# Kernel tuning notes

Hardware: AMD Instinct MI355X
Metric: run time of the kernel (lower is better)

## Reference

```python
import jax, jax.numpy as jnp
import numpy as np

B, T, E = 4, 2048, 1024
H = 16
HS = E // H  # head_size = d_model // num_heads, d_model == E here
D_FF = 4 * E
EPS = 1e-5


def _layernorm(x, g, b):
    mu = jnp.mean(x, axis=-1, keepdims=True)
    var = jnp.var(x, axis=-1, keepdims=True)
    return (x - mu) * jax.lax.rsqrt(var + EPS) * g + b


def setup_inputs() -> dict:
    key = jax.random.key(0)
    ks = jax.random.split(key, 12)
    s_e = 1.0 / np.sqrt(E)
    s_ff = 1.0 / np.sqrt(D_FF)
    return {
        "x": jax.random.normal(ks[0], (B, T, E), jnp.float32),
        "ln1_g": jnp.ones((E,), jnp.float32),
        "ln1_b": jnp.zeros((E,), jnp.float32),
        "Wq": jax.random.normal(ks[1], (E, E), jnp.float32) * s_e,
        "bq": jnp.zeros((E,), jnp.float32),
        "Wk": jax.random.normal(ks[2], (E, E), jnp.float32) * s_e,
        "bk": jnp.zeros((E,), jnp.float32),
        "Wv": jax.random.normal(ks[3], (E, E), jnp.float32) * s_e,
        "bv": jnp.zeros((E,), jnp.float32),
        "Wp": jax.random.normal(ks[4], (E, E), jnp.float32) * s_e,
        "bp": jnp.zeros((E,), jnp.float32),
        "ln2_g": jnp.ones((E,), jnp.float32),
        "ln2_b": jnp.zeros((E,), jnp.float32),
        "W1": jax.random.normal(ks[5], (E, D_FF), jnp.float32) * s_e,
        "b1": jnp.zeros((D_FF,), jnp.float32),
        "W2": jax.random.normal(ks[6], (D_FF, E), jnp.float32) * s_ff,
        "b2": jnp.zeros((E,), jnp.float32),
    }


def reference(x, ln1_g, ln1_b, Wq, bq, Wk, bk, Wv, bv, Wp, bp,
              ln2_g, ln2_b, W1, b1, W2, b2):
    # --- attention sublayer ---
    h = _layernorm(x, ln1_g, ln1_b)                      # [B,T,E]
    q = (h @ Wq + bq).reshape(B, T, H, HS)
    k = (h @ Wk + bk).reshape(B, T, H, HS)
    v = (h @ Wv + bv).reshape(B, T, H, HS)
    scores = jnp.einsum('bqhd,bkhd->bhqk', q, k) * (HS ** -0.5)  # [B,H,T,T]
    causal = jnp.tril(jnp.ones((T, T), bool))
    scores = jnp.where(causal, scores, -jnp.inf)
    w = jax.nn.softmax(scores, axis=-1)
    attn = jnp.einsum('bhqk,bkhd->bqhd', w, v).reshape(B, T, H * HS)
    x = x + attn @ Wp + bp
    # --- FFN sublayer ---
    h2 = _layernorm(x, ln2_g, ln2_b)
    x = x + jax.nn.relu(h2 @ W1 + b1) @ W2 + b2
    return x
```

## Files before the change

kernel.cpp:

```cpp
#include <hip/hip_runtime.h>
#include <hip/hip_bf16.h>

#define B_ 4
#define T_ 2048
#define E_ 1024
#define H_ 16
#define HS_ 64
#define DFF_ 4096
#define M_ (B_ * T_)
#define LDQ_ (3 * E_)

typedef __bf16 bf16_t;
typedef __bf16 bf16x4 __attribute__((ext_vector_type(4)));
typedef __bf16 bf16x8 __attribute__((ext_vector_type(8)));
typedef float f32x4 __attribute__((ext_vector_type(4)));

#define AS1 __attribute__((address_space(1)))
#define AS3 __attribute__((address_space(3)))

__device__ __forceinline__ void gload_lds16(const void* g, void* l) {
  __builtin_amdgcn_global_load_lds((AS1 void*)(g), (AS3 void*)(l), 16, 0, 0);
}

__global__ __launch_bounds__(256) void wtrans_kernel(
    const float* __restrict__ W, bf16_t* __restrict__ Wt, int Krows, int Ncols) {
  __shared__ float tile[32][33];
  int tx = threadIdx.x, ty = threadIdx.y;
  int n0 = blockIdx.x * 32, k0 = blockIdx.y * 32;
#pragma unroll
  for (int i = 0; i < 32; i += 8)
    tile[ty + i][tx] = W[(long)(k0 + ty + i) * Ncols + n0 + tx];
  __syncthreads();
#pragma unroll
  for (int i = 0; i < 32; i += 8)
    Wt[(long)(n0 + ty + i) * Krows + k0 + tx] = (bf16_t)tile[tx][ty + i];
}

__global__ __launch_bounds__(256) void bcat_kernel(const float* a, const float* b,
                                                   const float* c, float* o) {
  int i = blockIdx.x * 256 + threadIdx.x;
  o[i] = i < 1024 ? a[i] : (i < 2048 ? b[i - 1024] : c[i - 2048]);
}

__global__ __launch_bounds__(256) void layernorm_kernel(
    const float* __restrict__ in, const float* __restrict__ g,
    const float* __restrict__ b, bf16_t* __restrict__ out) {
  int row = blockIdx.x;
  int tid = threadIdx.x;
  const float4* inr = (const float4*)(in + (long)row * E_);
  float4 v = inr[tid];
  float s = v.x + v.y + v.z + v.w;
  float ss = v.x * v.x + v.y * v.y + v.z * v.z + v.w * v.w;
#pragma unroll
  for (int o = 32; o; o >>= 1) {
    s += __shfl_xor(s, o);
    ss += __shfl_xor(ss, o);
  }
  __shared__ float red[8];
  int wv = tid >> 6;
  if ((tid & 63) == 0) {
    red[wv] = s;
    red[4 + wv] = ss;
  }
  __syncthreads();
  s = red[0] + red[1] + red[2] + red[3];
  ss = red[4] + red[5] + red[6] + red[7];
  float mu = s * (1.f / E_);
  float var = ss * (1.f / E_) - mu * mu;
  float rs = rsqrtf(var + 1e-5f);
  int ci = tid * 4;
  float4 gv = *(const float4*)(g + ci);
  float4 bv = *(const float4*)(b + ci);
  long o0 = (long)row * E_ + ci;
  out[o0 + 0] = (bf16_t)((v.x - mu) * rs * gv.x + bv.x);
  out[o0 + 1] = (bf16_t)((v.y - mu) * rs * gv.y + bv.y);
  out[o0 + 2] = (bf16_t)((v.z - mu) * rs * gv.z + bv.z);
  out[o0 + 3] = (bf16_t)((v.w - mu) * rs * gv.w + bv.w);
}

template <int MODE>
__global__ __launch_bounds__(256, 2) void gemm_bt_kernel(
    const bf16_t* __restrict__ A, const bf16_t* __restrict__ Bt,
    const float* __restrict__ bias, const float* __restrict__ resid,
    void* __restrict__ out, int N, int K) {
  __shared__ bf16_t As[2][128 * 64];
  __shared__ bf16_t Bs[2][128 * 64];
  const int tid = threadIdx.x;
  const int lane = tid & 63;
  const int wave = tid >> 6;
  const int wr = wave >> 1, wc = wave & 1;
  const int quad = lane >> 4, l16 = lane & 15;
  const int id = blockIdx.y * gridDim.x + blockIdx.x;
  const int xcd = id & 7;
  const int k_ = id >> 3;
  const int bxr = k_ % gridDim.x;
  const int byr = (k_ / gridDim.x) * 8 + xcd;
  const long rowBase = (long)byr * 128;
  const long colBase = (long)bxr * 128;

  f32x4 acc[4][4] = {};

  auto stage = [&](int buf, int k0) {
#pragma unroll
    for (int i = 0; i < 4; ++i) {
      int c = i * 256 + tid;
      int row = c >> 3;
      int gcol = ((c & 7) ^ (row & 7)) * 8;
      gload_lds16(&A[(rowBase + row) * K + k0 + gcol],
                  &As[buf][(i * 256 + wave * 64) * 8]);
      gload_lds16(&Bt[(colBase + row) * K + k0 + gcol],
                  &Bs[buf][(i * 256 + wave * 64) * 8]);
    }
  };

  stage(0, 0);
  __syncthreads();

  for (int k0 = 0; k0 < K; k0 += 64) {
    const int cur = (k0 >> 6) & 1;
    if (k0 + 64 < K) stage(cur ^ 1, k0 + 64);
#pragma unroll
    for (int kk = 0; kk < 2; ++kk) {
      bf16x8 af[4], bfr[4];
#pragma unroll
      for (int i = 0; i < 4; ++i) {
        int rowA = wr * 64 + i * 16 + l16;
        af[i] = *(const bf16x8*)&As[cur][(rowA * 8 + ((quad + 4 * kk) ^ (rowA & 7))) * 8];
        int rowB = wc * 64 + i * 16 + l16;
        bfr[i] = *(const bf16x8*)&Bs[cur][(rowB * 8 + ((quad + 4 * kk) ^ (rowB & 7))) * 8];
      }
#pragma unroll
      for (int mi = 0; mi < 4; ++mi)
#pragma unroll
        for (int ni = 0; ni < 4; ++ni)
          acc[mi][ni] = __builtin_amdgcn_mfma_f32_16x16x32_bf16(
              af[mi], bfr[ni], acc[mi][ni], 0, 0, 0);
    }
    __syncthreads();
  }

#pragma unroll
  for (int mi = 0; mi < 4; ++mi) {
#pragma unroll
    for (int ni = 0; ni < 4; ++ni) {
      int colg = (int)colBase + wc * 64 + ni * 16 + l16;
      float bv = bias[colg];
#pragma unroll
      for (int r = 0; r < 4; ++r) {
        long rowg = rowBase + wr * 64 + mi * 16 + quad * 4 + r;
        float v = acc[mi][ni][r] + bv;
        long idx = rowg * N + colg;
        if (MODE == 0) {
          ((bf16_t*)out)[idx] = (bf16_t)v;
        } else if (MODE == 1) {
          ((float*)out)[idx] = v + resid[idx];
        } else {
          ((bf16_t*)out)[idx] = (bf16_t)fmaxf(v, 0.f);
        }
      }
    }
  }
}

__global__ __launch_bounds__(256) void vtrans_kernel(
    const bf16_t* __restrict__ qkv, bf16_t* __restrict__ vt) {
  __shared__ bf16_t tile[32][33];
  int tx = threadIdx.x, ty = threadIdx.y;
  int t0 = blockIdx.x * 32;
  int d0 = (blockIdx.y & 1) * 32;
  int bh = blockIdx.y >> 1;
  int b = bh >> 4, hh = bh & 15;
#pragma unroll
  for (int i = 0; i < 32; i += 8)
    tile[ty + i][tx] =
        qkv[(long)(b * T_ + t0 + ty + i) * LDQ_ + 2 * E_ + hh * HS_ + d0 + tx];
  __syncthreads();
#pragma unroll
  for (int i = 0; i < 32; i += 8)
    vt[((long)bh * HS_ + d0 + ty + i) * T_ + t0 + tx] = tile[tx][ty + i];
}

__global__ __launch_bounds__(256) void flash_attn_kernel(
    const bf16_t* __restrict__ qkv, const bf16_t* __restrict__ vt,
    bf16_t* __restrict__ attn, bf16_t* __restrict__ Opart,
    float* __restrict__ mlpart) {
  int gx = blockIdx.x;
  int ti = 0, sp = 0;
  for (int t = 0; t < 16; ++t) {
    int ns = t / 6 + 1;
    if (gx < ns) { ti = t; sp = gx; break; }
    gx -= ns;
  }
  const int nsplit = ti / 6 + 1;
  const int totIt = 2 * (ti + 1);
  const int jbeg = 12 * sp;
  const int jend = min(jbeg + 12, totIt);

  const int tid = threadIdx.x;
  const int lane = tid & 63, wave = tid >> 6;
  const int quad = lane >> 4, l16 = lane & 15;
  const int bh = blockIdx.y, b = bh >> 4, hh = bh & 15;
  const int q0 = ti * 128;
  const int qw = q0 + wave * 32;

  __shared__ __align__(16) bf16_t Ks[64][72];
  __shared__ __align__(16) bf16_t Vs[64][72];
  __shared__ __align__(16) bf16_t Ps[4][16][72];

  const bf16_t* qb = qkv;
  const bf16_t* kb = qkv + E_;

  bf16x8 aq[2][2];
#pragma unroll
  for (int s = 0; s < 2; ++s) {
    long base = (long)(b * T_ + qw + s * 16 + l16) * LDQ_ + hh * HS_ + quad * 8;
    aq[s][0] = *(const bf16x8*)&qb[base];
    aq[s][1] = *(const bf16x8*)&qb[base + 32];
#pragma unroll
    for (int e = 0; e < 8; ++e) {
      aq[s][0][e] = (bf16_t)((float)aq[s][0][e] * 0.125f);
      aq[s][1][e] = (bf16_t)((float)aq[s][1][e] * 0.125f);
    }
  }

  f32x4 o[2][4] = {};
  float lsum[2] = {};

  const int srow = tid >> 3;
  const int scol = (tid & 7) * 8;

  for (int j = jbeg; j < jend; ++j) {
    int kv0 = j * 64;
#pragma unroll
    for (int p = 0; p < 2; ++p) {
      int row = p * 32 + srow;
      *(uint4*)&Ks[row][scol] =
          *(const uint4*)&kb[(long)(b * T_ + kv0 + row) * LDQ_ + hh * HS_ + scol];
      *(uint4*)&Vs[row][scol] =
          *(const uint4*)&vt[((long)bh * HS_ + row) * T_ + kv0 + scol];
    }
    __syncthreads();

#pragma unroll
    for (int s = 0; s < 2; ++s) {
      int qs = qw + s * 16;
      if (kv0 <= qs + 15) {
        f32x4 sc[4];
#pragma unroll
        for (int sub = 0; sub < 4; ++sub) {
          f32x4 t = {};
          t = __builtin_amdgcn_mfma_f32_16x16x32_bf16(
              *(const bf16x8*)&Ks[sub * 16 + l16][quad * 8], aq[s][0], t, 0, 0, 0);
          t = __builtin_amdgcn_mfma_f32_16x16x32_bf16(
              *(const bf16x8*)&Ks[sub * 16 + l16][32 + quad * 8], aq[s][1], t, 0, 0, 0);
          sc[sub] = t;
        }
        if (kv0 + 63 > qs) {
          int qcol = qs + l16;
#pragma unroll
          for (int sub = 0; sub < 4; ++sub)
#pragma unroll
            for (int r = 0; r < 4; ++r) {
              int kvrow = kv0 + sub * 16 + quad * 4 + r;
              if (kvrow > qcol) sc[sub][r] = -INFINITY;
            }
        }
        float part = 0.f;
#pragma unroll
        for (int sub = 0; sub < 4; ++sub) {
#pragma unroll
          for (int r = 0; r < 4; ++r) sc[sub][r] = __expf(sc[sub][r]);
          part += (sc[sub][0] + sc[sub][1]) + (sc[sub][2] + sc[sub][3]);
        }
        lsum[s] += part;
#pragma unroll
        for (int sub = 0; sub < 4; ++sub) {
          bf16x4 pk;
#pragma unroll
          for (int r = 0; r < 4; ++r) pk[r] = (bf16_t)sc[sub][r];
          *(bf16x4*)&Ps[wave][l16][sub * 16 + quad * 4] = pk;
        }
        bf16x8 ap0 = *(const bf16x8*)&Ps[wave][l16][quad * 8];
        bf16x8 ap1 = *(const bf16x8*)&Ps[wave][l16][32 + quad * 8];
#pragma unroll
        for (int nt = 0; nt < 4; ++nt) {
          o[s][nt] = __builtin_amdgcn_mfma_f32_16x16x32_bf16(
              *(const bf16x8*)&Vs[nt * 16 + l16][quad * 8], ap0, o[s][nt], 0, 0, 0);
          o[s][nt] = __builtin_amdgcn_mfma_f32_16x16x32_bf16(
              *(const bf16x8*)&Vs[nt * 16 + l16][32 + quad * 8], ap1, o[s][nt], 0, 0, 0);
        }
      }
    }
    __syncthreads();
  }

  float lval[2];
#pragma unroll
  for (int s = 0; s < 2; ++s) {
    float v = lsum[s];
    v += __shfl_xor(v, 16);
    v += __shfl_xor(v, 32);
    lval[s] = v;
  }

  if (nsplit == 1) {
#pragma unroll
    for (int s = 0; s < 2; ++s) {
      float inv = 1.f / lval[s];
      long rowg = (long)b * T_ + qw + s * 16 + l16;
#pragma unroll
      for (int nt = 0; nt < 4; ++nt) {
        bf16x4 pk;
#pragma unroll
        for (int r = 0; r < 4; ++r) pk[r] = (bf16_t)(o[s][nt][r] * inv);
        *(bf16x4*)&attn[rowg * E_ + hh * HS_ + nt * 16 + quad * 4] = pk;
      }
    }
  } else {
    int idx = (ti < 12) ? (ti - 6) * 2 + sp : 12 + (ti - 12) * 3 + sp;
    long slot = (long)bh * 24 + idx;
    bf16_t* op = Opart + slot * (128 * 64);
    float* ml = mlpart + slot * 256;
#pragma unroll
    for (int s = 0; s < 2; ++s) {
      float inv = 1.f / lval[s];
      int rloc = wave * 32 + s * 16 + l16;
#pragma unroll
      for (int nt = 0; nt < 4; ++nt) {
        bf16x4 pk;
#pragma unroll
        for (int r = 0; r < 4; ++r) pk[r] = (bf16_t)(o[s][nt][r] * inv);
        *(bf16x4*)&op[rloc * 64 + nt * 16 + quad * 4] = pk;
      }
      if (quad == 0) ml[rloc] = lval[s];
    }
  }
}

__global__ __launch_bounds__(256) void flash_merge_kernel(
    const bf16_t* __restrict__ Opart, const float* __restrict__ mlpart,
    bf16_t* __restrict__ attn) {
  int ti = 6 + blockIdx.x;
  int bh = blockIdx.y, b = bh >> 4, hh = bh & 15;
  int ns = ti / 6 + 1;
  int base_idx = (ti < 12) ? (ti - 6) * 2 : 12 + (ti - 12) * 3;
  int r = threadIdx.x >> 1;
  int dh = (threadIdx.x & 1) * 32;

  float w[3], den = 0.f;
  for (int s = 0; s < ns; ++s) {
    long slot = (long)bh * 24 + base_idx + s;
    w[s] = mlpart[slot * 256 + r];
    den += w[s];
  }
  float inv = 1.f / den;
  float acc[32];
#pragma unroll
  for (int d = 0; d < 32; ++d) acc[d] = 0.f;
  for (int s = 0; s < ns; ++s) {
    long slot = (long)bh * 24 + base_idx + s;
    const bf16_t* op = Opart + slot * (128 * 64) + r * 64 + dh;
#pragma unroll
    for (int d = 0; d < 32; ++d) acc[d] += w[s] * (float)op[d];
  }
  long rowg = (long)b * T_ + ti * 128 + r;
  bf16_t* dst = attn + rowg * E_ + hh * HS_ + dh;
#pragma unroll
  for (int d = 0; d < 32; ++d) dst[d] = (bf16_t)(acc[d] * inv);
}

extern "C" void kernel_launch(void* const* d_in, const int* in_sizes, int n_in,
                              void* d_out, int out_size, void* d_ws,
                              size_t ws_size, hipStream_t stream) {
  const float* x = (const float*)d_in[0];
  const float* ln1_g = (const float*)d_in[1];
  const float* ln1_b = (const float*)d_in[2];
  const float* Wq = (const float*)d_in[3];
  const float* bq = (const float*)d_in[4];
  const float* Wk = (const float*)d_in[5];
  const float* bk = (const float*)d_in[6];
  const float* Wv = (const float*)d_in[7];
  const float* bv = (const float*)d_in[8];
  const float* Wp = (const float*)d_in[9];
  const float* bp = (const float*)d_in[10];
  const float* ln2_g = (const float*)d_in[11];
  const float* ln2_b = (const float*)d_in[12];
  const float* W1 = (const float*)d_in[13];
  const float* b1 = (const float*)d_in[14];
  const float* W2 = (const float*)d_in[15];
  const float* b2 = (const float*)d_in[16];
  float* out = (float*)d_out;

  const size_t MB = 1ull << 20;
  char* ws = (char*)d_ws;
  bf16_t* wqkvt = (bf16_t*)(ws + 0 * MB);
  bf16_t* wpt   = (bf16_t*)(ws + 6 * MB);
  bf16_t* w1t   = (bf16_t*)(ws + 8 * MB);
  bf16_t* w2t   = (bf16_t*)(ws + 16 * MB);
  float*  bqkv  = (float*)(ws + 24 * MB);
  bf16_t* h     = (bf16_t*)(ws + 25 * MB);
  bf16_t* qkvb  = (bf16_t*)(ws + 41 * MB);
  bf16_t* vt    = (bf16_t*)(ws + 89 * MB);
  float*  xmid  = (float*)(ws + 105 * MB);
  bf16_t* Opart = (bf16_t*)(ws + 105 * MB);
  float* mlpart = (float*)(ws + 131 * MB);
  bf16_t* attn  = h;
  bf16_t* h2    = h;
  bf16_t* ff1   = qkvb;

  dim3 tb(32, 8);
  wtrans_kernel<<<dim3(E_ / 32, E_ / 32), tb, 0, stream>>>(Wq, wqkvt, E_, E_);
  wtrans_kernel<<<dim3(E_ / 32, E_ / 32), tb, 0, stream>>>(Wk, wqkvt + (long)E_ * E_, E_, E_);
  wtrans_kernel<<<dim3(E_ / 32, E_ / 32), tb, 0, stream>>>(Wv, wqkvt + 2l * E_ * E_, E_, E_);
  wtrans_kernel<<<dim3(E_ / 32, E_ / 32), tb, 0, stream>>>(Wp, wpt, E_, E_);
  wtrans_kernel<<<dim3(DFF_ / 32, E_ / 32), tb, 0, stream>>>(W1, w1t, E_, DFF_);
  wtrans_kernel<<<dim3(E_ / 32, DFF_ / 32), tb, 0, stream>>>(W2, w2t, DFF_, E_);
  bcat_kernel<<<12, 256, 0, stream>>>(bq, bk, bv, bqkv);

  layernorm_kernel<<<M_, 256, 0, stream>>>(x, ln1_g, ln1_b, h);

  gemm_bt_kernel<0><<<dim3(3 * E_ / 128, M_ / 128), 256, 0, stream>>>(
      h, wqkvt, bqkv, nullptr, qkvb, 3 * E_, E_);

  vtrans_kernel<<<dim3(T_ / 32, 2 * B_ * H_), tb, 0, stream>>>(qkvb, vt);

  flash_attn_kernel<<<dim3(30, B_ * H_), 256, 0, stream>>>(qkvb, vt, attn,
                                                           Opart, mlpart);
  flash_merge_kernel<<<dim3(10, B_ * H_), 256, 0, stream>>>(Opart, mlpart, attn);

  gemm_bt_kernel<1><<<dim3(E_ / 128, M_ / 128), 256, 0, stream>>>(
      attn, wpt, bp, x, xmid, E_, E_);

  layernorm_kernel<<<M_, 256, 0, stream>>>(xmid, ln2_g, ln2_b, h2);

  gemm_bt_kernel<2><<<dim3(DFF_ / 128, M_ / 128), 256, 0, stream>>>(
      h2, w1t, b1, nullptr, ff1, DFF_, E_);
  gemm_bt_kernel<1><<<dim3(E_ / 128, M_ / 128), 256, 0, stream>>>(
      ff1, w2t, b2, xmid, out, E_, DFF_);
}
```

Baseline: 495.8 us.

## Double-buffer K/V tiles with async global-to-LDS loads and XOR swizzle

```diff
diff --git a/kernel.cpp b/kernel.cpp
--- a/kernel.cpp
+++ b/kernel.cpp
@@ -203,13 +203,14 @@
   const int q0 = ti * 128;
   const int qw = q0 + wave * 32;
 
-  __shared__ __align__(16) bf16_t Ks[64][72];
-  __shared__ __align__(16) bf16_t Vs[64][72];
+  __shared__ __align__(16) bf16_t Ks[2][64 * 64];
+  __shared__ __align__(16) bf16_t Vs[2][64 * 64];
   __shared__ __align__(16) bf16_t Ps[4][16][72];
 
   const bf16_t* qb = qkv;
   const bf16_t* kb = qkv + E_;
 
+  const float QSC = 0.125f * 1.44269504f;
   bf16x8 aq[2][2];
 #pragma unroll
   for (int s = 0; s < 2; ++s) {
@@ -218,28 +219,36 @@
     aq[s][1] = *(const bf16x8*)&qb[base + 32];
 #pragma unroll
     for (int e = 0; e < 8; ++e) {
-      aq[s][0][e] = (bf16_t)((float)aq[s][0][e] * 0.125f);
-      aq[s][1][e] = (bf16_t)((float)aq[s][1][e] * 0.125f);
+      aq[s][0][e] = (bf16_t)((float)aq[s][0][e] * QSC);
+      aq[s][1][e] = (bf16_t)((float)aq[s][1][e] * QSC);
     }
   }
 
   f32x4 o[2][4] = {};
   float lsum[2] = {};
 
-  const int srow = tid >> 3;
-  const int scol = (tid & 7) * 8;
+  auto stageKV = [&](int buf, int kv0) {
+#pragma unroll
+    for (int i = 0; i < 2; ++i) {
+      int c = i * 256 + tid;
+      int row = c >> 3;
+      int col = ((c & 7) ^ (row & 7)) * 8;
+      gload_lds16(&kb[(long)(b * T_ + kv0 + row) * LDQ_ + hh * HS_ + col],
+                  &Ks[buf][(i * 256 + wave * 64) * 8]);
+      gload_lds16(&vt[((long)bh * HS_ + row) * T_ + kv0 + col],
+                  &Vs[buf][(i * 256 + wave * 64) * 8]);
+    }
+  };
+
+  stageKV(0, jbeg * 64);
+  __syncthreads();
 
   for (int j = jbeg; j < jend; ++j) {
     int kv0 = j * 64;
-#pragma unroll
-    for (int p = 0; p < 2; ++p) {
-      int row = p * 32 + srow;
-      *(uint4*)&Ks[row][scol] =
-          *(const uint4*)&kb[(long)(b * T_ + kv0 + row) * LDQ_ + hh * HS_ + scol];
-      *(uint4*)&Vs[row][scol] =
-          *(const uint4*)&vt[((long)bh * HS_ + row) * T_ + kv0 + scol];
-    }
-    __syncthreads();
+    const int cur = (j - jbeg) & 1;
+    if (j + 1 < jend) stageKV(cur ^ 1, (j + 1) * 64);
+    const bf16_t* Kc = &Ks[cur][0];
+    const bf16_t* Vc = &Vs[cur][0];
 
 #pragma unroll
     for (int s = 0; s < 2; ++s) {
@@ -248,11 +257,14 @@
         f32x4 sc[4];
 #pragma unroll
         for (int sub = 0; sub < 4; ++sub) {
+          int rowK = sub * 16 + l16;
           f32x4 t = {};
           t = __builtin_amdgcn_mfma_f32_16x16x32_bf16(
-              *(const bf16x8*)&Ks[sub * 16 + l16][quad * 8], aq[s][0], t, 0, 0, 0);
+              *(const bf16x8*)&Kc[(rowK * 8 + (quad ^ (rowK & 7))) * 8],
+              aq[s][0], t, 0, 0, 0);
           t = __builtin_amdgcn_mfma_f32_16x16x32_bf16(
-              *(const bf16x8*)&Ks[sub * 16 + l16][32 + quad * 8], aq[s][1], t, 0, 0, 0);
+              *(const bf16x8*)&Kc[(rowK * 8 + ((4 + quad) ^ (rowK & 7))) * 8],
+              aq[s][1], t, 0, 0, 0);
           sc[sub] = t;
         }
         if (kv0 + 63 > qs) {
@@ -269,7 +281,7 @@
 #pragma unroll
         for (int sub = 0; sub < 4; ++sub) {
 #pragma unroll
-          for (int r = 0; r < 4; ++r) sc[sub][r] = __expf(sc[sub][r]);
+          for (int r = 0; r < 4; ++r) sc[sub][r] = exp2f(sc[sub][r]);
           part += (sc[sub][0] + sc[sub][1]) + (sc[sub][2] + sc[sub][3]);
         }
         lsum[s] += part;
@@ -284,10 +296,13 @@
         bf16x8 ap1 = *(const bf16x8*)&Ps[wave][l16][32 + quad * 8];
 #pragma unroll
         for (int nt = 0; nt < 4; ++nt) {
+          int rowV = nt * 16 + l16;
           o[s][nt] = __builtin_amdgcn_mfma_f32_16x16x32_bf16(
-              *(const bf16x8*)&Vs[nt * 16 + l16][quad * 8], ap0, o[s][nt], 0, 0, 0);
+              *(const bf16x8*)&Vc[(rowV * 8 + (quad ^ (rowV & 7))) * 8],
+              ap0, o[s][nt], 0, 0, 0);
           o[s][nt] = __builtin_amdgcn_mfma_f32_16x16x32_bf16(
-              *(const bf16x8*)&Vs[nt * 16 + l16][32 + quad * 8], ap1, o[s][nt], 0, 0, 0);
+              *(const bf16x8*)&Vc[(rowV * 8 + ((4 + quad) ^ (rowV & 7))) * 8],
+              ap1, o[s][nt], 0, 0, 0);
         }
       }
     }
```

Result: no change. 496.1 us (+0.1%).
